# Kernel tuning notes

Measured on AMD Instinct MI355X. Metric: run time of the kernel, lower is better.

## Reference

```python
import jax, jax.numpy as jnp
import numpy as np

D_MODEL = 1024
N_HEADS = 16
D_HEAD = D_MODEL // N_HEADS
LUT_SIZE = 4096
TWO_PI = 2.0 * np.pi
SCALE = np.sqrt(2.0 * D_HEAD).astype(np.float32)

# Global sin/cos lookup table over [0, 2*pi), 4096 entries (mirrors get_global_lut(4096)).
_GRID = (TWO_PI * np.arange(LUT_SIZE) / LUT_SIZE).astype(np.float32)
_SIN_TABLE = jnp.asarray(np.sin(_GRID))
_COS_TABLE = jnp.asarray(np.cos(_GRID))


def _lut_sin_cos(theta):
    # quantize angle to nearest LUT bin (wrap mod 2*pi) and gather
    idx = jnp.mod(jnp.round(theta * (LUT_SIZE / TWO_PI)).astype(jnp.int32), LUT_SIZE)
    return _SIN_TABLE[idx], _COS_TABLE[idx]


def setup_inputs() -> dict:
    key = jax.random.key(0)
    ks = jax.random.split(key, 7)
    B, S = 2, 2048
    x = jax.random.normal(ks[0], (B, S, D_MODEL), dtype=jnp.float32)
    w_q = 0.02 * jax.random.normal(ks[1], (N_HEADS, D_HEAD), dtype=jnp.float32)
    b_q = jnp.zeros((N_HEADS, D_HEAD), dtype=jnp.float32)
    w_k = 0.02 * jax.random.normal(ks[2], (N_HEADS, D_HEAD), dtype=jnp.float32)
    b_k = jnp.zeros((N_HEADS, D_HEAD), dtype=jnp.float32)
    v_w = jax.random.normal(ks[3], (D_MODEL, D_MODEL), dtype=jnp.float32) / np.sqrt(D_MODEL)
    out_w = jax.random.normal(ks[4], (D_MODEL, D_MODEL), dtype=jnp.float32) / np.sqrt(D_MODEL)
    return {"x": x, "w_q": w_q, "b_q": b_q, "w_k": w_k, "b_k": b_k, "v_w": v_w, "out_w": out_w}


def reference(x, w_q, b_q, w_k, b_k, v_w, out_w):
    B, S, D = x.shape
    x_heads = x.reshape(B, S, N_HEADS, D_HEAD)

    theta_q = x_heads / (1.0 + jnp.abs(w_q)) + b_q          # (B,S,H,dh)
    sin_q, cos_q = _lut_sin_cos(theta_q)
    Q = jnp.concatenate([cos_q, sin_q], axis=-1)            # (B,S,H,2dh)

    theta_k = x_heads / (1.0 + jnp.abs(w_k)) + b_k
    sin_k, cos_k = _lut_sin_cos(theta_k)
    K = jnp.concatenate([cos_k, sin_k], axis=-1)            # (B,S,H,2dh)

    V = (x @ v_w.T).reshape(B, S, N_HEADS, D_HEAD)          # (B,S,H,dh)

    scores = jnp.einsum("bqhe,bkhe->bhqk", Q, K) / SCALE    # (B,H,S,S)
    causal = jnp.triu(jnp.ones((S, S), dtype=bool), k=1)
    scores = jnp.where(causal, -jnp.inf, scores)
    attn = jax.nn.softmax(scores, axis=-1)

    out = jnp.einsum("bhqk,bkhd->bqhd", attn, V).reshape(B, S, D)
    return out @ out_w.T
```

## Files before the change

kernel.cpp:

```cpp
#include <hip/hip_runtime.h>
#include <hip/hip_bf16.h>
#include <math.h>


typedef __attribute__((ext_vector_type(8))) __bf16 bf16x8;
typedef __attribute__((ext_vector_type(4))) __bf16 bf16x4;
typedef __attribute__((ext_vector_type(4))) float f32x4;
typedef unsigned short ushort_t;
typedef unsigned int uint_t;

#define LUTC 651.8986469044033f
#define ANG 0.0015339807878856412f
#define QSCL 0.12751743590489435f

__device__ __forceinline__ float fast_exp2(float x) {
#if __has_builtin(__builtin_amdgcn_exp2f)
  return __builtin_amdgcn_exp2f(x);
#else
  return exp2f(x);
#endif
}

__device__ __forceinline__ ushort_t f2bf(float f) {
  union { __bf16 b; ushort_t u; } cv;
  cv.b = (__bf16)f;
  return cv.u;
}

__device__ __forceinline__ float bf2f(ushort_t u) {
  union { float f; uint_t u; } cv;
  cv.u = ((uint_t)u) << 16;
  return cv.f;
}

__device__ __forceinline__ void store8(ushort_t* p, const ushort_t v[8]) {
  uint4 u;
  u.x = (uint_t)v[0] | ((uint_t)v[1] << 16);
  u.y = (uint_t)v[2] | ((uint_t)v[3] << 16);
  u.z = (uint_t)v[4] | ((uint_t)v[5] << 16);
  u.w = (uint_t)v[6] | ((uint_t)v[7] << 16);
  *(uint4*)p = u;
}

__device__ __forceinline__ void gl_lds16(const void* g, void* l) {
  __builtin_amdgcn_global_load_lds(
      (__attribute__((address_space(1))) void*)(g),
      (__attribute__((address_space(3))) void*)(l),
      16, 0, 0);
}

__global__ __launch_bounds__(256) void prep_kernel(
    const float* __restrict__ x, const float* __restrict__ wq, const float* __restrict__ bq,
    const float* __restrict__ wk, const float* __restrict__ bk,
    ushort_t* __restrict__ Qs, ushort_t* __restrict__ Ks, ushort_t* __restrict__ xb)
{
  int t = blockIdx.x * 256 + threadIdx.x;
  int dm8 = t & 127;
  int g = t >> 7;
  int dm0 = dm8 * 8;
  int h = dm0 >> 6;

  float aq[8], cq[8], ak[8], ck[8];
#pragma unroll
  for (int j = 0; j < 8; ++j) {
    aq[j] = LUTC / (1.0f + fabsf(wq[dm0 + j]));
    cq[j] = LUTC * bq[dm0 + j];
    ak[j] = LUTC / (1.0f + fabsf(wk[dm0 + j]));
    ck[j] = LUTC * bk[dm0 + j];
  }
  for (int i = 0; i < 4; ++i) {
    int bs = g * 4 + i;
    int b = bs >> 11, s = bs & 2047;
    const float4* xp4 = (const float4*)(x + (size_t)bs * 1024 + dm0);
    float4 xa = xp4[0], xbv4 = xp4[1];
    float xv[8] = {xa.x, xa.y, xa.z, xa.w, xbv4.x, xbv4.y, xbv4.z, xbv4.w};
    ushort_t qc[8], qs[8], kc[8], ks[8], xo[8];
#pragma unroll
    for (int j = 0; j < 8; ++j) {
      int iq = ((int)rintf(fmaf(xv[j], aq[j], cq[j]))) & 4095;
      float sq, cqv;
      __sincosf((float)iq * ANG, &sq, &cqv);
      int ik = ((int)rintf(fmaf(xv[j], ak[j], ck[j]))) & 4095;
      float sk, ckv;
      __sincosf((float)ik * ANG, &sk, &ckv);
      qc[j] = f2bf(cqv * QSCL);
      qs[j] = f2bf(sq * QSCL);
      kc[j] = f2bf(ckv);
      ks[j] = f2bf(sk);
      xo[j] = f2bf(xv[j]);
    }
    size_t qb = ((size_t)(b * 16 + h) * 2048 + s) * 128 + (dm0 & 63);
    store8(Qs + qb, qc);        store8(Qs + qb + 64, qs);
    store8(Ks + qb, kc);        store8(Ks + qb + 64, ks);
    store8(xb + (size_t)bs * 1024 + dm0, xo);
  }
}

__global__ __launch_bounds__(256) void wconv_kernel(
    const float* __restrict__ vw, const float* __restrict__ ow,
    ushort_t* __restrict__ vwb, ushort_t* __restrict__ owb)
{
  int t = blockIdx.x * 256 + threadIdx.x;
  const float* src;
  ushort_t* dst;
  int i;
  if (t < 131072) { src = vw; dst = vwb; i = t; }
  else            { src = ow; dst = owb; i = t - 131072; }
  const float4* p4 = (const float4*)(src + (size_t)i * 8);
  float4 a = p4[0], b = p4[1];
  float v[8] = {a.x, a.y, a.z, a.w, b.x, b.y, b.z, b.w};
  ushort_t o[8];
#pragma unroll
  for (int j = 0; j < 8; ++j) o[j] = f2bf(v[j]);
  store8(dst + (size_t)i * 8, o);
}

template <int EPI>
__global__ __launch_bounds__(256) void gemm_nt(
    const ushort_t* __restrict__ A, const ushort_t* __restrict__ B,
    float* __restrict__ Cf, ushort_t* __restrict__ Cb, int M, int N, int K)
{
  __shared__ __align__(16) ushort_t As[2][64 * 64];
  __shared__ __align__(16) ushort_t Bs[2][128 * 64];
  const int l = threadIdx.x & 63;
  const int w = threadIdx.x >> 6;
  const int g = l >> 4, lo = l & 15;
  const int mt = blockIdx.x % (M >> 6);
  const int nt = blockIdx.x / (M >> 6);
  const int m0 = mt << 6, n0 = nt << 7;

  const f32x4 zero4 = {0.f, 0.f, 0.f, 0.f};
  f32x4 acc[4][2];
#pragma unroll
  for (int i = 0; i < 4; ++i)
#pragma unroll
    for (int j = 0; j < 2; ++j) acc[i][j] = zero4;

  const int nk = K >> 6;

#define GEMM_STAGE(buf, k0_)                                                    \
  {                                                                             \
    int k0__ = (k0_);                                                           \
    _Pragma("unroll")                                                           \
    for (int i = 0; i < 2; ++i) {                                               \
      int ci = (w * 2 + i) * 64 + l;                                            \
      int r = ci >> 3, c = (ci & 7) ^ (r & 7);                                  \
      gl_lds16(A + (size_t)(m0 + r) * K + k0__ + c * 8, &As[buf][(w * 2 + i) * 512]); \
    }                                                                           \
    _Pragma("unroll")                                                           \
    for (int i = 0; i < 4; ++i) {                                               \
      int ci = (w * 4 + i) * 64 + l;                                            \
      int r = ci >> 3, c = (ci & 7) ^ (r & 7);                                  \
      gl_lds16(B + (size_t)(n0 + r) * K + k0__ + c * 8, &Bs[buf][(w * 4 + i) * 512]); \
    }                                                                           \
  }

  GEMM_STAGE(0, 0);
  GEMM_STAGE(1, 64);
  asm volatile("s_waitcnt vmcnt(6)" ::: "memory");
  __builtin_amdgcn_s_barrier();
  __builtin_amdgcn_sched_barrier(0);

  for (int t = 0; t < nk; ++t) {
    int cb = t & 1;
#pragma unroll
    for (int kk = 0; kk < 2; ++kk) {
      bf16x8 af[4], bfr[2];
#pragma unroll
      for (int mi = 0; mi < 4; ++mi) {
        int r = mi * 16 + lo;
        int ch = (g + 4 * kk) ^ (r & 7);
        af[mi] = *(const bf16x8*)&As[cb][r * 64 + ch * 8];
      }
#pragma unroll
      for (int ni = 0; ni < 2; ++ni) {
        int r = w * 32 + ni * 16 + lo;
        int ch = (g + 4 * kk) ^ (r & 7);
        bfr[ni] = *(const bf16x8*)&Bs[cb][r * 64 + ch * 8];
      }
#pragma unroll
      for (int mi = 0; mi < 4; ++mi)
#pragma unroll
        for (int ni = 0; ni < 2; ++ni)
          acc[mi][ni] = __builtin_amdgcn_mfma_f32_16x16x32_bf16(af[mi], bfr[ni], acc[mi][ni], 0, 0, 0);
    }
    __builtin_amdgcn_sched_barrier(0);
    asm volatile("s_waitcnt lgkmcnt(0)" ::: "memory");
    __builtin_amdgcn_s_barrier();
    if (t + 2 < nk) {
      GEMM_STAGE(cb, (t + 2) * 64);
      asm volatile("s_waitcnt vmcnt(6)" ::: "memory");
    } else {
      asm volatile("s_waitcnt vmcnt(0)" ::: "memory");
    }
    __builtin_amdgcn_s_barrier();
    __builtin_amdgcn_sched_barrier(0);
  }
#undef GEMM_STAGE

#pragma unroll
  for (int mi = 0; mi < 4; ++mi)
#pragma unroll
    for (int ni = 0; ni < 2; ++ni)
#pragma unroll
      for (int reg = 0; reg < 4; ++reg) {
        int row = m0 + mi * 16 + g * 4 + reg;
        int col = n0 + w * 32 + ni * 16 + lo;
        float v = acc[mi][ni][reg];
        if (EPI == 0) {
          Cf[(size_t)row * N + col] = v;
        } else {
          size_t o = (size_t)(col >> 11) * (1024 * 2048) + (size_t)row * 2048 + (col & 2047);
          Cb[o] = f2bf(v);
        }
      }
}


template<bool MASKED>
__device__ __forceinline__ void attn_tile(
    const ushort_t* __restrict__ Kc, const ushort_t* __restrict__ Vc,
    const bf16x8 (&qf)[2][4], f32x4 (&accO)[2][4], f32x4 (&acc_l)[2],
    int kb, int qw, int lo, int g, const bf16x8& ones)
{
  const f32x4 zero4 = {0.f, 0.f, 0.f, 0.f};
  f32x4 sc[2][4];
#pragma unroll
  for (int qm = 0; qm < 2; ++qm)
#pragma unroll
    for (int ns = 0; ns < 4; ++ns) sc[qm][ns] = zero4;

#pragma unroll
  for (int e = 0; e < 4; ++e) {
#pragma unroll
    for (int ns = 0; ns < 4; ++ns) {
      int kr = ns * 16 + lo;
      int cc = (g + 4 * e) ^ (kr & 7);
      bf16x8 kf = *(const bf16x8*)&Kc[kr * 128 + cc * 8];
#pragma unroll
      for (int qm = 0; qm < 2; ++qm)
        sc[qm][ns] = __builtin_amdgcn_mfma_f32_16x16x32_bf16(kf, qf[qm][e], sc[qm][ns], 0, 0, 0);
    }
  }

  bf16x8 pa[2][2];
#pragma unroll
  for (int qm = 0; qm < 2; ++qm) {
#pragma unroll
    for (int ns = 0; ns < 4; ++ns) {
#pragma unroll
      for (int reg = 0; reg < 4; ++reg) {
        float sv = sc[qm][ns][reg];
        if (MASKED) {
          int ka = kb + ns * 16 + g * 4 + reg;
          int qa = qw + qm * 16 + lo;
          sv = (ka <= qa) ? sv : -__builtin_inff();
        }
        pa[qm][ns >> 1][(ns & 1) * 4 + reg] = (__bf16)fast_exp2(sv);
      }
    }
  }

#pragma unroll
  for (int kk = 0; kk < 2; ++kk) {
#pragma unroll
    for (int nd = 0; nd < 4; ++nd) {
      int vr = nd * 16 + lo;
      int h8 = (g & 1) * 4;
      int cc0 = (4 * kk + (g >> 1)) ^ (vr & 7);
      int cc1 = (4 * kk + 2 + (g >> 1)) ^ (vr & 7);
      union { bf16x8 v8; bf16x4 v4[2]; } u;
      u.v4[0] = *(const bf16x4*)&Vc[vr * 64 + cc0 * 8 + h8];
      u.v4[1] = *(const bf16x4*)&Vc[vr * 64 + cc1 * 8 + h8];
#pragma unroll
      for (int qm = 0; qm < 2; ++qm)
        accO[qm][nd] = __builtin_amdgcn_mfma_f32_16x16x32_bf16(pa[qm][kk], u.v8, accO[qm][nd], 0, 0, 0);
    }
#pragma unroll
    for (int qm = 0; qm < 2; ++qm)
      acc_l[qm] = __builtin_amdgcn_mfma_f32_16x16x32_bf16(pa[qm][kk], ones, acc_l[qm], 0, 0, 0);
  }
}

__global__ __launch_bounds__(256) void attn_kernel(
    const ushort_t* __restrict__ Qs, const ushort_t* __restrict__ Ks,
    const ushort_t* __restrict__ Vt, ushort_t* __restrict__ Ob,
    ushort_t* __restrict__ pnB, float* __restrict__ plA, float* __restrict__ plB)
{
  const int S = 2048;
  const int id = blockIdx.x;
  const int bh = id & 31;
  const int seg = id >> 5;
  int qt, k0, ntl, mode;
  if (seg < 8)       { qt = 7 - seg;  k0 = 0;      ntl = 2 * qt + 2; mode = 0; }
  else if (seg < 16) { qt = seg;      k0 = 0;      ntl = qt + 1;     mode = 1; }
  else               { qt = seg - 8;  k0 = qt + 1; ntl = qt + 1;     mode = 2; }
  const int p = bh * 8 + (qt - 8);

  const int l = threadIdx.x & 63;
  const int w = threadIdx.x >> 6;
  const int g = l >> 4, lo = l & 15;

  __shared__ __align__(16) ushort_t Kl[2][64 * 128];
  __shared__ __align__(16) ushort_t Vl[2][64 * 64];

  const int qw = qt * 128 + w * 32;
  const ushort_t* Kbase = Ks + (size_t)bh * S * 128;
  const ushort_t* Vbase = Vt + (size_t)bh * 64 * S;

  bf16x8 ones;
#pragma unroll
  for (int j = 0; j < 8; ++j) ones[j] = (__bf16)1.0f;

  bf16x8 qf[2][4];
#pragma unroll
  for (int qm = 0; qm < 2; ++qm) {
    const ushort_t* qp = Qs + ((size_t)bh * S + qw + qm * 16 + lo) * 128 + 8 * g;
#pragma unroll
    for (int e = 0; e < 4; ++e) qf[qm][e] = *(const bf16x8*)(qp + 32 * e);
  }

  const f32x4 zero4 = {0.f, 0.f, 0.f, 0.f};
  f32x4 accO[2][4];
  f32x4 acc_l[2];
#pragma unroll
  for (int qm = 0; qm < 2; ++qm) {
    acc_l[qm] = zero4;
#pragma unroll
    for (int nd = 0; nd < 4; ++nd) accO[qm][nd] = zero4;
  }

#define ATTN_STAGE(buf, kb_)                                                    \
  {                                                                             \
    int kb__ = (kb_);                                                           \
    _Pragma("unroll")                                                           \
    for (int i = 0; i < 4; ++i) {                                               \
      int ci = (w * 4 + i) * 64 + l;                                            \
      int r = ci >> 4, c = (ci & 15) ^ (r & 7);                                 \
      gl_lds16(Kbase + (size_t)(kb__ + r) * 128 + c * 8, &Kl[buf][(w * 4 + i) * 512]); \
    }                                                                           \
    _Pragma("unroll")                                                           \
    for (int i = 0; i < 2; ++i) {                                               \
      int ci = (w * 2 + i) * 64 + l;                                            \
      int r = ci >> 3, c = (ci & 7) ^ (r & 7);                                  \
      gl_lds16(Vbase + (size_t)r * S + kb__ + c * 8, &Vl[buf][(w * 2 + i) * 512]); \
    }                                                                           \
  }

  ATTN_STAGE(0, k0 * 64);
  ATTN_STAGE(1, (k0 + 1) * 64);
  asm volatile("s_waitcnt vmcnt(6)" ::: "memory");
  __builtin_amdgcn_s_barrier();
  __builtin_amdgcn_sched_barrier(0);

  for (int t = 0; t < ntl; ++t) {
    int cb = t & 1;
    int gt = k0 + t;
    __builtin_amdgcn_s_setprio(1);
    if (gt < 2 * qt)
      attn_tile<false>(Kl[cb], Vl[cb], qf, accO, acc_l, gt * 64, qw, lo, g, ones);
    else
      attn_tile<true>(Kl[cb], Vl[cb], qf, accO, acc_l, gt * 64, qw, lo, g, ones);
    __builtin_amdgcn_s_setprio(0);
    __builtin_amdgcn_sched_barrier(0);
    asm volatile("s_waitcnt lgkmcnt(0)" ::: "memory");
    __builtin_amdgcn_s_barrier();
    if (t + 2 < ntl) {
      ATTN_STAGE(cb, (gt + 2) * 64);
      asm volatile("s_waitcnt vmcnt(6)" ::: "memory");
    } else {
      asm volatile("s_waitcnt vmcnt(0)" ::: "memory");
    }
    __builtin_amdgcn_s_barrier();
    __builtin_amdgcn_sched_barrier(0);
  }
#undef ATTN_STAGE

  const int b = bh >> 4, h = bh & 15;
  if (mode == 0) {
    float linv[2][4];
#pragma unroll
    for (int qm = 0; qm < 2; ++qm)
#pragma unroll
      for (int reg = 0; reg < 4; ++reg)
        linv[qm][reg] = 1.0f / acc_l[qm][reg];
#pragma unroll
    for (int qm = 0; qm < 2; ++qm)
#pragma unroll
      for (int nd = 0; nd < 4; ++nd)
#pragma unroll
        for (int reg = 0; reg < 4; ++reg) {
          int q = qw + qm * 16 + g * 4 + reg;
          int d = nd * 16 + lo;
          Ob[((size_t)(b * 2048 + q)) * 1024 + h * 64 + d] = f2bf(accO[qm][nd][reg] * linv[qm][reg]);
        }
  } else if (mode == 1) {
#pragma unroll
    for (int qm = 0; qm < 2; ++qm) {
#pragma unroll
      for (int nd = 0; nd < 4; ++nd)
#pragma unroll
        for (int reg = 0; reg < 4; ++reg) {
          int q = qw + qm * 16 + g * 4 + reg;
          int d = nd * 16 + lo;
          Ob[((size_t)(b * 2048 + q)) * 1024 + h * 64 + d] = f2bf(accO[qm][nd][reg]);
        }
      if (lo == 0) {
#pragma unroll
        for (int reg = 0; reg < 4; ++reg)
          plA[p * 128 + w * 32 + qm * 16 + g * 4 + reg] = acc_l[qm][reg];
      }
    }
  } else {
#pragma unroll
    for (int qm = 0; qm < 2; ++qm) {
#pragma unroll
      for (int nd = 0; nd < 4; ++nd)
#pragma unroll
        for (int reg = 0; reg < 4; ++reg) {
          int qr = w * 32 + qm * 16 + g * 4 + reg;
          int d = nd * 16 + lo;
          pnB[((size_t)p * 128 + qr) * 64 + d] = f2bf(accO[qm][nd][reg]);
        }
      if (lo == 0) {
#pragma unroll
        for (int reg = 0; reg < 4; ++reg)
          plB[p * 128 + w * 32 + qm * 16 + g * 4 + reg] = acc_l[qm][reg];
      }
    }
  }
}

__global__ __launch_bounds__(256) void combine_kernel(
    ushort_t* __restrict__ Ob, const ushort_t* __restrict__ pnB,
    const float* __restrict__ plA, const float* __restrict__ plB)
{
  int t = blockIdx.x * 256 + threadIdx.x;
  int d0 = (t & 7) * 8;
  int qidx = t >> 3;
  int seg = qidx >> 7, qr = qidx & 127;
  int bh = seg >> 3, j = seg & 7;
  int qt = 8 + j;
  int b = bh >> 4, h = bh & 15;
  int qglob = qt * 128 + qr;

  ushort_t* op = Ob + ((size_t)(b * 2048 + qglob)) * 1024 + h * 64 + d0;
  const ushort_t* bp = pnB + ((size_t)seg * 128 + qr) * 64 + d0;
  uint4 ua = *(const uint4*)op;
  uint4 ub = *(const uint4*)bp;
  float inv = 1.0f / (plA[seg * 128 + qr] + plB[seg * 128 + qr]);

  const uint_t* pa = (const uint_t*)&ua;
  const uint_t* pb = (const uint_t*)&ub;
  ushort_t o[8];
#pragma unroll
  for (int i = 0; i < 4; ++i) {
    float a0 = bf2f((ushort_t)(pa[i] & 0xffff));
    float a1 = bf2f((ushort_t)(pa[i] >> 16));
    float b0 = bf2f((ushort_t)(pb[i] & 0xffff));
    float b1 = bf2f((ushort_t)(pb[i] >> 16));
    o[2 * i]     = f2bf((a0 + b0) * inv);
    o[2 * i + 1] = f2bf((a1 + b1) * inv);
  }
  store8(op, o);
}

extern "C" void kernel_launch(void* const* d_in, const int* in_sizes, int n_in,
                              void* d_out, int out_size, void* d_ws, size_t ws_size,
                              hipStream_t stream) {
  const float* x  = (const float*)d_in[0];
  const float* wq = (const float*)d_in[1];
  const float* bq = (const float*)d_in[2];
  const float* wk = (const float*)d_in[3];
  const float* bk = (const float*)d_in[4];
  const float* vw = (const float*)d_in[5];
  const float* ow = (const float*)d_in[6];
  float* out = (float*)d_out;

  char* ws = (char*)d_ws;
  ushort_t* Qs  = (ushort_t*)(ws);
  ushort_t* Ksb = (ushort_t*)(ws + (16u << 20));
  ushort_t* Vtb = (ushort_t*)(ws + (32u << 20));
  ushort_t* xbb = (ushort_t*)(ws + (40u << 20));
  ushort_t* Obb = (ushort_t*)(ws + (48u << 20));
  ushort_t* vwb = (ushort_t*)(ws + (56u << 20));
  ushort_t* owb = (ushort_t*)(ws + (58u << 20));

  ushort_t* pnB = (ushort_t*)(ws + (40u << 20));
  float*    plA = (float*)(ws + (40u << 20) + 4 * 1048576 + 262144);
  float*    plB = (float*)(ws + (40u << 20) + 4 * 1048576 + 524288);

  prep_kernel<<<512, 256, 0, stream>>>(x, wq, bq, wk, bk, Qs, Ksb, xbb);
  wconv_kernel<<<1024, 256, 0, stream>>>(vw, ow, vwb, owb);
  gemm_nt<1><<<512, 256, 0, stream>>>(vwb, xbb, nullptr, Vtb, 1024, 4096, 1024);
  attn_kernel<<<768, 256, 0, stream>>>(Qs, Ksb, Vtb, Obb, pnB, plA, plB);
  combine_kernel<<<1024, 256, 0, stream>>>(Obb, pnB, plA, plB);
  gemm_nt<0><<<512, 256, 0, stream>>>(Obb, owb, out, nullptr, 4096, 1024, 1024);
}
```

Baseline: 103.7 us.

## Merge weight conversion into prep, triple-buffer GEMM/attention, rebalance attention work split

```diff
diff --git a/kernel.cpp b/kernel.cpp
--- a/kernel.cpp
+++ b/kernel.cpp
@@ -52,8 +52,27 @@
 __global__ __launch_bounds__(256) void prep_kernel(
     const float* __restrict__ x, const float* __restrict__ wq, const float* __restrict__ bq,
     const float* __restrict__ wk, const float* __restrict__ bk,
-    ushort_t* __restrict__ Qs, ushort_t* __restrict__ Ks, ushort_t* __restrict__ xb)
+    ushort_t* __restrict__ Qs, ushort_t* __restrict__ Ks, ushort_t* __restrict__ xb,
+    const float* __restrict__ vw, const float* __restrict__ ow,
+    ushort_t* __restrict__ vwb, ushort_t* __restrict__ owb)
 {
+  if (blockIdx.x >= 512) {
+    int t = (blockIdx.x - 512) * 256 + threadIdx.x;
+    const float* src;
+    ushort_t* dst;
+    int i;
+    if (t < 131072) { src = vw; dst = vwb; i = t; }
+    else            { src = ow; dst = owb; i = t - 131072; }
+    const float4* p4 = (const float4*)(src + (size_t)i * 8);
+    float4 a = p4[0], b = p4[1];
+    float v[8] = {a.x, a.y, a.z, a.w, b.x, b.y, b.z, b.w};
+    ushort_t o[8];
+#pragma unroll
+    for (int j = 0; j < 8; ++j) o[j] = f2bf(v[j]);
+    store8(dst + (size_t)i * 8, o);
+    return;
+  }
+
   int t = blockIdx.x * 256 + threadIdx.x;
   int dm8 = t & 127;
   int g = t >> 7;
@@ -96,32 +115,13 @@
   }
 }
 
-__global__ __launch_bounds__(256) void wconv_kernel(
-    const float* __restrict__ vw, const float* __restrict__ ow,
-    ushort_t* __restrict__ vwb, ushort_t* __restrict__ owb)
-{
-  int t = blockIdx.x * 256 + threadIdx.x;
-  const float* src;
-  ushort_t* dst;
-  int i;
-  if (t < 131072) { src = vw; dst = vwb; i = t; }
-  else            { src = ow; dst = owb; i = t - 131072; }
-  const float4* p4 = (const float4*)(src + (size_t)i * 8);
-  float4 a = p4[0], b = p4[1];
-  float v[8] = {a.x, a.y, a.z, a.w, b.x, b.y, b.z, b.w};
-  ushort_t o[8];
-#pragma unroll
-  for (int j = 0; j < 8; ++j) o[j] = f2bf(v[j]);
-  store8(dst + (size_t)i * 8, o);
-}
-
 template <int EPI>
 __global__ __launch_bounds__(256) void gemm_nt(
     const ushort_t* __restrict__ A, const ushort_t* __restrict__ B,
     float* __restrict__ Cf, ushort_t* __restrict__ Cb, int M, int N, int K)
 {
-  __shared__ __align__(16) ushort_t As[2][64 * 64];
-  __shared__ __align__(16) ushort_t Bs[2][128 * 64];
+  __shared__ __align__(16) ushort_t As[3][64 * 64];
+  __shared__ __align__(16) ushort_t Bs[3][128 * 64];
   const int l = threadIdx.x & 63;
   const int w = threadIdx.x >> 6;
   const int g = l >> 4, lo = l & 15;
@@ -161,8 +161,8 @@
   __builtin_amdgcn_s_barrier();
   __builtin_amdgcn_sched_barrier(0);
 
+  int rb = 0, wb = 2;
   for (int t = 0; t < nk; ++t) {
-    int cb = t & 1;
 #pragma unroll
     for (int kk = 0; kk < 2; ++kk) {
       bf16x8 af[4], bfr[2];
@@ -170,13 +170,13 @@
       for (int mi = 0; mi < 4; ++mi) {
         int r = mi * 16 + lo;
         int ch = (g + 4 * kk) ^ (r & 7);
-        af[mi] = *(const bf16x8*)&As[cb][r * 64 + ch * 8];
+        af[mi] = *(const bf16x8*)&As[rb][r * 64 + ch * 8];
       }
 #pragma unroll
       for (int ni = 0; ni < 2; ++ni) {
         int r = w * 32 + ni * 16 + lo;
         int ch = (g + 4 * kk) ^ (r & 7);
-        bfr[ni] = *(const bf16x8*)&Bs[cb][r * 64 + ch * 8];
+        bfr[ni] = *(const bf16x8*)&Bs[rb][r * 64 + ch * 8];
       }
 #pragma unroll
       for (int mi = 0; mi < 4; ++mi)
@@ -185,16 +185,20 @@
           acc[mi][ni] = __builtin_amdgcn_mfma_f32_16x16x32_bf16(af[mi], bfr[ni], acc[mi][ni], 0, 0, 0);
     }
     __builtin_amdgcn_sched_barrier(0);
-    asm volatile("s_waitcnt lgkmcnt(0)" ::: "memory");
-    __builtin_amdgcn_s_barrier();
     if (t + 2 < nk) {
-      GEMM_STAGE(cb, (t + 2) * 64);
+      GEMM_STAGE(wb, (t + 2) * 64);
+      asm volatile("s_waitcnt lgkmcnt(0)" ::: "memory");
       asm volatile("s_waitcnt vmcnt(6)" ::: "memory");
-    } else {
+    } else if (t + 1 < nk) {
+      asm volatile("s_waitcnt lgkmcnt(0)" ::: "memory");
       asm volatile("s_waitcnt vmcnt(0)" ::: "memory");
     }
-    __builtin_amdgcn_s_barrier();
-    __builtin_amdgcn_sched_barrier(0);
+    if (t + 1 < nk) {
+      __builtin_amdgcn_s_barrier();
+      __builtin_amdgcn_sched_barrier(0);
+    }
+    rb = (rb == 2) ? 0 : rb + 1;
+    wb = (wb == 2) ? 0 : wb + 1;
   }
 #undef GEMM_STAGE
 
@@ -216,7 +220,6 @@
       }
 }
 
-
 template<bool MASKED>
 __device__ __forceinline__ void attn_tile(
     const ushort_t* __restrict__ Kc, const ushort_t* __restrict__ Vc,
@@ -282,6 +285,7 @@
   }
 }
 
+
 __global__ __launch_bounds__(256) void attn_kernel(
     const ushort_t* __restrict__ Qs, const ushort_t* __restrict__ Ks,
     const ushort_t* __restrict__ Vt, ushort_t* __restrict__ Ob,
@@ -290,45 +294,31 @@
   const int S = 2048;
   const int id = blockIdx.x;
   const int bh = id & 31;
-  const int seg = id >> 5;
-  int qt, k0, ntl, mode;
-  if (seg < 8)       { qt = 7 - seg;  k0 = 0;      ntl = 2 * qt + 2; mode = 0; }
-  else if (seg < 16) { qt = seg;      k0 = 0;      ntl = qt + 1;     mode = 1; }
-  else               { qt = seg - 8;  k0 = qt + 1; ntl = qt + 1;     mode = 2; }
-  const int p = bh * 8 + (qt - 8);
+  const int j = (id >> 5) & 7;
+  const int side = id >> 8;
+  const int qtH = 15 - j;
+  const int p = bh * 8 + j;
 
   const int l = threadIdx.x & 63;
   const int w = threadIdx.x >> 6;
   const int g = l >> 4, lo = l & 15;
 
-  __shared__ __align__(16) ushort_t Kl[2][64 * 128];
-  __shared__ __align__(16) ushort_t Vl[2][64 * 64];
-
-  const int qw = qt * 128 + w * 32;
+  __shared__ __align__(16) ushort_t Kl[3][64 * 128];
+  __shared__ __align__(16) ushort_t Vl[3][64 * 64];
+
   const ushort_t* Kbase = Ks + (size_t)bh * S * 128;
   const ushort_t* Vbase = Vt + (size_t)bh * 64 * S;
+  const int b = bh >> 4, h = bh & 15;
 
   bf16x8 ones;
 #pragma unroll
-  for (int j = 0; j < 8; ++j) ones[j] = (__bf16)1.0f;
+  for (int jj = 0; jj < 8; ++jj) ones[jj] = (__bf16)1.0f;
+  const f32x4 zero4 = {0.f, 0.f, 0.f, 0.f};
 
   bf16x8 qf[2][4];
-#pragma unroll
-  for (int qm = 0; qm < 2; ++qm) {
-    const ushort_t* qp = Qs + ((size_t)bh * S + qw + qm * 16 + lo) * 128 + 8 * g;
-#pragma unroll
-    for (int e = 0; e < 4; ++e) qf[qm][e] = *(const bf16x8*)(qp + 32 * e);
-  }
-
-  const f32x4 zero4 = {0.f, 0.f, 0.f, 0.f};
   f32x4 accO[2][4];
   f32x4 acc_l[2];
-#pragma unroll
-  for (int qm = 0; qm < 2; ++qm) {
-    acc_l[qm] = zero4;
-#pragma unroll
-    for (int nd = 0; nd < 4; ++nd) accO[qm][nd] = zero4;
-  }
+  int qw = 0;
 
 #define ATTN_STAGE(buf, kb_)                                                    \
   {                                                                             \
@@ -347,54 +337,64 @@
     }                                                                           \
   }
 
-  ATTN_STAGE(0, k0 * 64);
-  ATTN_STAGE(1, (k0 + 1) * 64);
-  asm volatile("s_waitcnt vmcnt(6)" ::: "memory");
-  __builtin_amdgcn_s_barrier();
-  __builtin_amdgcn_sched_barrier(0);
-
-  for (int t = 0; t < ntl; ++t) {
-    int cb = t & 1;
-    int gt = k0 + t;
-    __builtin_amdgcn_s_setprio(1);
-    if (gt < 2 * qt)
-      attn_tile<false>(Kl[cb], Vl[cb], qf, accO, acc_l, gt * 64, qw, lo, g, ones);
-    else
-      attn_tile<true>(Kl[cb], Vl[cb], qf, accO, acc_l, gt * 64, qw, lo, g, ones);
-    __builtin_amdgcn_s_setprio(0);
-    __builtin_amdgcn_sched_barrier(0);
-    asm volatile("s_waitcnt lgkmcnt(0)" ::: "memory");
-    __builtin_amdgcn_s_barrier();
-    if (t + 2 < ntl) {
-      ATTN_STAGE(cb, (gt + 2) * 64);
-      asm volatile("s_waitcnt vmcnt(6)" ::: "memory");
-    } else {
-      asm volatile("s_waitcnt vmcnt(0)" ::: "memory");
-    }
-    __builtin_amdgcn_s_barrier();
-    __builtin_amdgcn_sched_barrier(0);
-  }
-#undef ATTN_STAGE
-
-  const int b = bh >> 4, h = bh & 15;
-  if (mode == 0) {
-    float linv[2][4];
-#pragma unroll
-    for (int qm = 0; qm < 2; ++qm)
-#pragma unroll
-      for (int reg = 0; reg < 4; ++reg)
-        linv[qm][reg] = 1.0f / acc_l[qm][reg];
-#pragma unroll
-    for (int qm = 0; qm < 2; ++qm)
-#pragma unroll
-      for (int nd = 0; nd < 4; ++nd)
-#pragma unroll
-        for (int reg = 0; reg < 4; ++reg) {
-          int q = qw + qm * 16 + g * 4 + reg;
-          int d = nd * 16 + lo;
-          Ob[((size_t)(b * 2048 + q)) * 1024 + h * 64 + d] = f2bf(accO[qm][nd][reg] * linv[qm][reg]);
-        }
-  } else if (mode == 1) {
+#define RUN_RANGE(qt_, k0_, ns_)                                                \
+  {                                                                             \
+    const int qtc = (qt_);                                                      \
+    const int k0c = (k0_);                                                      \
+    const int nsc = (ns_);                                                      \
+    qw = qtc * 128 + w * 32;                                                    \
+    asm volatile("s_waitcnt lgkmcnt(0)" ::: "memory");                          \
+    __builtin_amdgcn_s_barrier();              \
+    _Pragma("unroll")                                                           \
+    for (int qm = 0; qm < 2; ++qm) {                                            \
+      const ushort_t* qp = Qs + ((size_t)bh * S + qw + qm * 16 + lo) * 128 + 8 * g; \
+      _Pragma("unroll")                                                         \
+      for (int e = 0; e < 4; ++e) qf[qm][e] = *(const bf16x8*)(qp + 32 * e);    \
+    }                                                                           \
+    _Pragma("unroll")                                                           \
+    for (int qm = 0; qm < 2; ++qm) {                                            \
+      acc_l[qm] = zero4;                                                        \
+      _Pragma("unroll")                                                         \
+      for (int nd = 0; nd < 4; ++nd) accO[qm][nd] = zero4;                      \
+    }                                                                           \
+    ATTN_STAGE(0, k0c * 64);                                                    \
+    if (nsc > 1) {                                                              \
+      ATTN_STAGE(1, (k0c + 1) * 64);                                            \
+      asm volatile("s_waitcnt vmcnt(6)" ::: "memory");                          \
+    } else {                                                                    \
+      asm volatile("s_waitcnt vmcnt(0)" ::: "memory");                          \
+    }                                                                           \
+    __builtin_amdgcn_s_barrier();                                               \
+    __builtin_amdgcn_sched_barrier(0);                                          \
+    int rb = 0, wb = 2;                                                         \
+    for (int t = 0; t < nsc; ++t) {                                             \
+      int gt = k0c + t;                                                         \
+      __builtin_amdgcn_s_setprio(1);                                            \
+      if (gt < 2 * qtc)                                                         \
+        attn_tile<false>(Kl[rb], Vl[rb], qf, accO, acc_l, gt * 64, qw, lo, g, ones); \
+      else                                                                      \
+        attn_tile<true>(Kl[rb], Vl[rb], qf, accO, acc_l, gt * 64, qw, lo, g, ones);  \
+      __builtin_amdgcn_s_setprio(0);                                            \
+      __builtin_amdgcn_sched_barrier(0);                                        \
+      if (t + 2 < nsc) {                                                        \
+        ATTN_STAGE(wb, (gt + 2) * 64);                                          \
+        asm volatile("s_waitcnt lgkmcnt(0)" ::: "memory");                      \
+        asm volatile("s_waitcnt vmcnt(6)" ::: "memory");                        \
+      } else if (t + 1 < nsc) {                                                 \
+        asm volatile("s_waitcnt lgkmcnt(0)" ::: "memory");                      \
+        asm volatile("s_waitcnt vmcnt(0)" ::: "memory");                        \
+      }                                                                         \
+      if (t + 1 < nsc) {                                                        \
+        __builtin_amdgcn_s_barrier();                                           \
+        __builtin_amdgcn_sched_barrier(0);                                      \
+      }                                                                         \
+      rb = (rb == 2) ? 0 : rb + 1;                                              \
+      wb = (wb == 2) ? 0 : wb + 1;                                              \
+    }                                                                           \
+  }
+
+  if (side == 0) {
+    RUN_RANGE(qtH, 0, 17);
 #pragma unroll
     for (int qm = 0; qm < 2; ++qm) {
 #pragma unroll
@@ -412,6 +412,7 @@
       }
     }
   } else {
+    RUN_RANGE(qtH, 17, 15 - 2 * j);
 #pragma unroll
     for (int qm = 0; qm < 2; ++qm) {
 #pragma unroll
@@ -428,7 +429,26 @@
           plB[p * 128 + w * 32 + qm * 16 + g * 4 + reg] = acc_l[qm][reg];
       }
     }
-  }
+    RUN_RANGE(j, 0, 2 * j + 2);
+    float linv[2][4];
+#pragma unroll
+    for (int qm = 0; qm < 2; ++qm)
+#pragma unroll
+      for (int reg = 0; reg < 4; ++reg)
+        linv[qm][reg] = 1.0f / acc_l[qm][reg];
+#pragma unroll
+    for (int qm = 0; qm < 2; ++qm)
+#pragma unroll
+      for (int nd = 0; nd < 4; ++nd)
+#pragma unroll
+        for (int reg = 0; reg < 4; ++reg) {
+          int q = qw + qm * 16 + g * 4 + reg;
+          int d = nd * 16 + lo;
+          Ob[((size_t)(b * 2048 + q)) * 1024 + h * 64 + d] = f2bf(accO[qm][nd][reg] * linv[qm][reg]);
+        }
+  }
+#undef RUN_RANGE
+#undef ATTN_STAGE
 }
 
 __global__ __launch_bounds__(256) void combine_kernel(
@@ -440,9 +460,9 @@
   int qidx = t >> 3;
   int seg = qidx >> 7, qr = qidx & 127;
   int bh = seg >> 3, j = seg & 7;
-  int qt = 8 + j;
+  int qtH = 15 - j;
   int b = bh >> 4, h = bh & 15;
-  int qglob = qt * 128 + qr;
+  int qglob = qtH * 128 + qr;
 
   ushort_t* op = Ob + ((size_t)(b * 2048 + qglob)) * 1024 + h * 64 + d0;
   const ushort_t* bp = pnB + ((size_t)seg * 128 + qr) * 64 + d0;
@@ -490,10 +510,10 @@
   float*    plA = (float*)(ws + (40u << 20) + 4 * 1048576 + 262144);
   float*    plB = (float*)(ws + (40u << 20) + 4 * 1048576 + 524288);
 
-  prep_kernel<<<512, 256, 0, stream>>>(x, wq, bq, wk, bk, Qs, Ksb, xbb);
-  wconv_kernel<<<1024, 256, 0, stream>>>(vw, ow, vwb, owb);
+  prep_kernel<<<1536, 256, 0, stream>>>(x, wq, bq, wk, bk, Qs, Ksb, xbb,
+                                        vw, ow, vwb, owb);
   gemm_nt<1><<<512, 256, 0, stream>>>(vwb, xbb, nullptr, Vtb, 1024, 4096, 1024);
-  attn_kernel<<<768, 256, 0, stream>>>(Qs, Ksb, Vtb, Obb, pnB, plA, plB);
+  attn_kernel<<<512, 256, 0, stream>>>(Qs, Ksb, Vtb, Obb, pnB, plA, plB);
   combine_kernel<<<1024, 256, 0, stream>>>(Obb, pnB, plA, plB);
   gemm_nt<0><<<512, 256, 0, stream>>>(Obb, owb, out, nullptr, 4096, 1024, 1024);
 }
```

New measurement: 100.1 us. -3.5%, faster.
